# Performance work log

Measured on AMD Instinct MI355X. Metric: run time of the kernel, lower is better.

The kernel has to match this reference:

```python
import jax, jax.numpy as jnp
import numpy as np

T, B, A, H = 128, 32, 6, 128  # rollout len, envs, actions, lstm hidden


def _conv(x, w, b, stride):
    # x: NCHW, w: OIHW (torch layout), VALID padding like nn.Conv2d default
    y = jax.lax.conv_general_dilated(
        x, w, (stride, stride), 'VALID',
        dimension_numbers=('NCHW', 'OIHW', 'NCHW'))
    return y + b[None, :, None, None]


def setup_inputs() -> dict:
    key = jax.random.key(0)
    ks = jax.random.split(key, 12)
    s = 0.05  # weight scale to keep activations in a sane range
    inp = {
        'x': jax.random.uniform(ks[0], (T * B, 1, 84, 84), jnp.float32) * 255.0,
        'done': (jax.random.uniform(ks[1], (T * B,)) < 0.05).astype(jnp.float32),
        'h0': jnp.zeros((1, B, H), jnp.float32),
        'c0': jnp.zeros((1, B, H), jnp.float32),
        'W1': jax.random.normal(ks[2], (32, 1, 8, 8), jnp.float32) * s,
        'b1': jnp.zeros((32,), jnp.float32),
        'W2': jax.random.normal(ks[3], (64, 32, 4, 4), jnp.float32) * s,
        'b2': jnp.zeros((64,), jnp.float32),
        'W3': jax.random.normal(ks[4], (64, 64, 3, 3), jnp.float32) * s,
        'b3': jnp.zeros((64,), jnp.float32),
        'Wfc': jax.random.normal(ks[5], (512, 3136), jnp.float32) * s,
        'bfc': jnp.zeros((512,), jnp.float32),
        'W_ih': jax.random.normal(ks[6], (4 * H, 512), jnp.float32) * s,
        'W_hh': jax.random.normal(ks[7], (4 * H, H), jnp.float32) * s,
        'b_ih': jnp.zeros((4 * H,), jnp.float32),
        'b_hh': jnp.zeros((4 * H,), jnp.float32),
        'Wa': jax.random.normal(ks[8], (A, H), jnp.float32) * 0.01,
        'ba': jnp.zeros((A,), jnp.float32),
        'Wc': jax.random.normal(ks[9], (1, H), jnp.float32) * s,
        'bc': jnp.zeros((1,), jnp.float32),
    }
    return inp


def reference(x, done, h0, c0, W1, b1, W2, b2, W3, b3, Wfc, bfc,
              W_ih, W_hh, b_ih, b_hh, Wa, ba, Wc, bc):
    # --- conv feature extractor (x / 255.0) ---
    z = x / 255.0
    z = jax.nn.relu(_conv(z, W1, b1, 4))   # (N,32,20,20)
    z = jax.nn.relu(_conv(z, W2, b2, 2))   # (N,64,9,9)
    z = jax.nn.relu(_conv(z, W3, b3, 1))   # (N,64,7,7)
    z = z.reshape(z.shape[0], -1)           # (N,3136), torch flatten order
    hidden = jax.nn.relu(z @ Wfc.T + bfc)   # (N,512)

    batch = h0.shape[1]
    xs = hidden.reshape(-1, batch, 512)     # (T,B,512)
    ds = done.reshape(-1, batch)            # (T,B)

    # precompute input projection for all steps at once
    gates_x = jnp.einsum('tbi,gi->tbg', xs, W_ih) + b_ih  # (T,B,4H)

    def step(carry, inp):
        h, c = carry
        gx, d = inp
        mask = (1.0 - d)[:, None]           # reset state where done
        h = h * mask
        c = c * mask
        gates = gx + h @ W_hh.T + b_hh
        i, f, g, o = jnp.split(gates, 4, axis=-1)  # torch gate order i,f,g,o
        c = jax.nn.sigmoid(f) * c + jax.nn.sigmoid(i) * jnp.tanh(g)
        h = jax.nn.sigmoid(o) * jnp.tanh(c)
        return (h, c), h

    (hT, cT), hs = jax.lax.scan(step, (h0[0], c0[0]), (gates_x, ds))
    new_hidden = hs.reshape(-1, hs.shape[-1])  # (T*B, 128)

    logits = new_hidden @ Wa.T + ba            # (T*B, A)
    value = new_hidden @ Wc.T + bc             # (T*B, 1)
    return logits, value, hT[None], cT[None]
```

## Files before the change

### kernel.cpp

```cpp
#include <hip/hip_runtime.h>

#define TT 128
#define BB 32
#define NN (TT*BB)

typedef float f4 __attribute__((ext_vector_type(4)));
typedef float f32x4 __attribute__((ext_vector_type(4)));
typedef short s8 __attribute__((ext_vector_type(8)));
typedef short bf16x8 __attribute__((ext_vector_type(8)));
typedef short s4v __attribute__((ext_vector_type(4)));

__device__ __forceinline__ float bf2f(unsigned short u){
  union{unsigned int i; float f;} x; x.i = ((unsigned int)u)<<16; return x.f;
}
__device__ __forceinline__ unsigned short f2bf(float f){
  union{float ff; unsigned int i;} x; x.ff=f;
  unsigned int r = x.i + 0x7FFFu + ((x.i>>16)&1u);
  return (unsigned short)(r>>16);
}
__device__ __forceinline__ float fsig(float x){
  return __builtin_amdgcn_rcpf(1.f + __expf(-x));
}
__device__ __forceinline__ float ftanh(float x){
  return 1.f - 2.f*__builtin_amdgcn_rcpf(1.f + __expf(2.f*x));
}
__device__ __forceinline__ void gload_lds16(const void* g, void* lds){
  __builtin_amdgcn_global_load_lds(
    (const __attribute__((address_space(1))) unsigned int*)g,
    (__attribute__((address_space(3))) unsigned int*)lds, 16, 0, 0);
}

__global__ __launch_bounds__(256) void prep_w1(const float* __restrict__ W1,
    unsigned short* __restrict__ w1c){
  int i = blockIdx.x*256 + threadIdx.x;
  w1c[i] = f2bf(W1[i] * (1.f/255.f));
}
__global__ __launch_bounds__(256) void prep_w2(const float* __restrict__ W2,
    unsigned short* __restrict__ w2c){
  int i = blockIdx.x*256 + threadIdx.x;
  int co = i >> 9; int rem = i & 511; int khw = rem >> 5; int ci = rem & 31;
  w2c[i] = f2bf(W2[(co*32 + ci)*16 + khw]);
}
__global__ __launch_bounds__(256) void prep_w3(const float* __restrict__ W3,
    unsigned short* __restrict__ w3c){
  int i = blockIdx.x*256 + threadIdx.x;
  int co = i/576; int rem = i - co*576; int khw = rem >> 6; int ci = rem & 63;
  w3c[i] = f2bf(W3[(co*64 + ci)*9 + khw]);
}
__global__ __launch_bounds__(256) void prep_wfc(const float* __restrict__ Wfc,
    unsigned short* __restrict__ wfcc){
  int i = blockIdx.x*256 + threadIdx.x;
  int nn = i/3136; int rem = i - nn*3136; int sp = rem >> 6; int ci = rem & 63;
  wfcc[i] = f2bf(Wfc[nn*3136 + ci*49 + sp]);
}
__global__ __launch_bounds__(256) void prep_wih(const float* __restrict__ W_ih,
    unsigned short* __restrict__ wihc){
  int i = blockIdx.x*256 + threadIdx.x;
  wihc[i] = f2bf(W_ih[i]);
}
__global__ __launch_bounds__(256) void prep_whh(const float* __restrict__ W_hh,
    unsigned short* __restrict__ whhc){
  int i = blockIdx.x*256 + threadIdx.x;
  whhc[i] = f2bf(W_hh[i]);
}

__global__ __launch_bounds__(256) void conv12_k(
    const float* __restrict__ x,
    const unsigned short* __restrict__ w1c, const float* __restrict__ b1,
    const unsigned short* __restrict__ w2c, const float* __restrict__ b2,
    unsigned short* __restrict__ z2){
  __shared__ unsigned short xI[84*88];
  __shared__ unsigned short z1s[200*64];
  __shared__ unsigned short w1L[32*68];
  int t = threadIdx.x;
  int n = blockIdx.x;
  int w = t >> 6, l = t & 63;
  int lr = l & 15, lg = l >> 4;

  {
    bf16x8 v = *(const bf16x8*)&w1c[t*8];
    *(bf16x8*)&w1L[(t>>3)*68 + (t&7)*8] = v;
  }
  {
    const float* xb = x + (size_t)n*7056;
    #pragma unroll
    for(int j=0;j<7;j++){
      int idx = t + 256*j;
      if(idx < 1764){
        f4 v = *(const f4*)(xb + idx*4);
        s4v p;
        #pragma unroll
        for(int e=0;e<4;e++) p[e] = (short)f2bf(v[e]);
        int row = idx/21, col = (idx - row*21)*4;
        *(s4v*)&xI[row*88 + col] = p;
      }
    }
  }
  __syncthreads();

  bf16x8 wf1[2][2];
  #pragma unroll
  for(int nt=0;nt<2;nt++)
    #pragma unroll
    for(int s=0;s<2;s++)
      wf1[nt][s] = *(const bf16x8*)&w1L[(nt*16+lr)*68 + s*32 + lg*8];
  f4 b1v[2];
  b1v[0] = *(const f4*)&b1[lg*4];
  b1v[1] = *(const f4*)&b1[16 + lg*4];
  for(int mt=w; mt<25; mt+=4){
    int p = mt*16 + lr;
    int oh = p/20, ow = p - oh*20;
    bf16x8 a0 = *(const bf16x8*)&xI[(oh*4 + lg    )*88 + ow*4];
    bf16x8 a1 = *(const bf16x8*)&xI[(oh*4 + 4 + lg)*88 + ow*4];
    f32x4 acc[2] = {};
    acc[0] = __builtin_amdgcn_mfma_f32_16x16x32_bf16(wf1[0][0], a0, acc[0], 0,0,0);
    acc[0] = __builtin_amdgcn_mfma_f32_16x16x32_bf16(wf1[0][1], a1, acc[0], 0,0,0);
    acc[1] = __builtin_amdgcn_mfma_f32_16x16x32_bf16(wf1[1][0], a0, acc[1], 0,0,0);
    acc[1] = __builtin_amdgcn_mfma_f32_16x16x32_bf16(wf1[1][1], a1, acc[1], 0,0,0);
    int row = p >> 1;
    int par = (p & 1) << 6;
    int swz = (row & 7) << 4;
    #pragma unroll
    for(int nt=0;nt<2;nt++){
      s4v hp;
      #pragma unroll
      for(int reg=0;reg<4;reg++){
        float v = acc[nt][reg] + b1v[nt][reg];
        v = v>0.f ? v : 0.f;
        hp[reg] = (short)f2bf(v);
      }
      int byteoff = (par + (nt*16 + lg*4)*2) ^ swz;
      *(s4v*)((char*)z1s + row*128 + byteoff) = hp;
    }
  }
  __syncthreads();

  int rbase[6];
  #pragma unroll
  for(int mt=0;mt<6;mt++){
    int q = mt*16 + lr; if(q > 80) q = 80;
    int oh = q/9, ow = q - oh*9;
    rbase[mt] = (2*oh)*20 + 2*ow;
  }
  const unsigned short* wrow = w2c + (size_t)(w*16 + lr)*512 + lg*8;
  bf16x8 bq0 = *(const bf16x8*)(wrow);
  bf16x8 bq1 = *(const bf16x8*)(wrow + 32);
  f32x4 acc2[6] = {};
  #pragma unroll
  for(int s=0;s<16;s++){
    bf16x8 bcur = (s & 1) ? bq1 : bq0;
    if(s+2 < 16){
      bf16x8 bn = *(const bf16x8*)(wrow + (s+2)*32);
      if(s & 1) bq1 = bn; else bq0 = bn;
    }
    int kh = s>>2, kw = s&3;
    int swzbase = ((kw & 1) << 6) + (lg << 4);
    #pragma unroll
    for(int mt=0;mt<6;mt++){
      int p = rbase[mt] + kh*20 + kw;
      int row = p >> 1;
      int byteoff = swzbase ^ ((row & 7) << 4);
      bf16x8 af = *(const bf16x8*)((const char*)z1s + row*128 + byteoff);
      acc2[mt] = __builtin_amdgcn_mfma_f32_16x16x32_bf16(af, bcur, acc2[mt], 0,0,0);
    }
  }
  {
    int ch = w*16 + lr;
    float bb = b2[ch];
    #pragma unroll
    for(int mt=0;mt<6;mt++)
      #pragma unroll
      for(int reg=0;reg<4;reg++){
        int q = mt*16 + lg*4 + reg;
        if(q < 81){
          float v = acc2[mt][reg] + bb; v = v>0.f ? v : 0.f;
          z2[((size_t)n*81 + q)*64 + ch] = f2bf(v);
        }
      }
  }
}

template<int MODE, int OUTBF16, int RELU, int SWZ>
__global__ __launch_bounds__(256) void mgemm_k(
    const unsigned short* __restrict__ A, const unsigned short* __restrict__ B,
    const float* __restrict__ bias1, const float* __restrict__ bias2,
    void* __restrict__ Cout, int K, int Nld, int nout){
  __shared__ unsigned short As[128*40];
  __shared__ unsigned short Bs[64*40];
  int t = threadIdx.x;
  int bm = blockIdx.y, bn = blockIdx.x;
  if(SWZ){
    int cpx = gridDim.y >> 3;
    bm = (bm & 7)*cpx + (bm >> 3);
  }
  int arow = t >> 1, ahalf = t & 1;
  int gm = bm*128 + arow;
  const unsigned short* abase;
  if(MODE == 0){
    abase = A + (size_t)gm*K + ahalf*16;
  } else {
    int n = gm/49; int r = gm - n*49; int oh = r/7; int ow = r - oh*7;
    abase = A + (((size_t)n*9 + oh)*9 + ow)*64 + ahalf*16;
  }
  int brow = t >> 2, bq = t & 3;
  const unsigned short* bbase = B + (size_t)(bn*64 + brow)*K + bq*8;
  int l = t & 63, w = t >> 6;
  int wr = w >> 1, wc = w & 1;
  int lr = l & 15, lk = (l >> 4)*8;
  f32x4 acc[4][2] = {};
  int nsteps = K >> 5;
  for(int s=0; s<nsteps; s++){
    const unsigned short* src;
    if(MODE == 0){
      src = abase + s*32;
    } else {
      int khw = s >> 1; int kh = khw/3; int kw = khw - kh*3;
      src = abase + (kh*9 + kw)*64 + (s & 1)*32;
    }
    bf16x8 a0 = *(const bf16x8*)src;
    bf16x8 a1 = *(const bf16x8*)(src + 8);
    *(bf16x8*)&As[arow*40 + ahalf*16] = a0;
    *(bf16x8*)&As[arow*40 + ahalf*16 + 8] = a1;
    bf16x8 bv = *(const bf16x8*)(bbase + s*32);
    *(bf16x8*)&Bs[brow*40 + bq*8] = bv;
    __syncthreads();
    bf16x8 af[4];
    #pragma unroll
    for(int mf=0; mf<4; mf++)
      af[mf] = *(const bf16x8*)&As[(wr*64 + mf*16 + lr)*40 + lk];
    bf16x8 b0 = *(const bf16x8*)&Bs[(wc*32 + lr)*40 + lk];
    bf16x8 b1 = *(const bf16x8*)&Bs[(wc*32 + 16 + lr)*40 + lk];
    #pragma unroll
    for(int mf=0; mf<4; mf++){
      acc[mf][0] = __builtin_amdgcn_mfma_f32_16x16x32_bf16(af[mf], b0, acc[mf][0], 0, 0, 0);
      acc[mf][1] = __builtin_amdgcn_mfma_f32_16x16x32_bf16(af[mf], b1, acc[mf][1], 0, 0, 0);
    }
    __syncthreads();
  }
  #pragma unroll
  for(int nf=0; nf<2; nf++){
    int gcol = bn*64 + wc*32 + nf*16 + lr;
    if(gcol >= nout) continue;
    float bb = bias1[gcol] + (bias2 ? bias2[gcol] : 0.f);
    #pragma unroll
    for(int mf=0; mf<4; mf++){
      #pragma unroll
      for(int reg=0; reg<4; reg++){
        int grow = bm*128 + wr*64 + mf*16 + (l>>4)*4 + reg;
        float v = acc[mf][nf][reg] + bb;
        if(RELU) v = v>0.f ? v : 0.f;
        if(OUTBF16) ((unsigned short*)Cout)[(size_t)grow*Nld + gcol] = f2bf(v);
        else        ((float*)Cout)[(size_t)grow*Nld + gcol] = v;
      }
    }
  }
}

__global__ __launch_bounds__(512) void lstm_v3_k(
    const float* __restrict__ gx,
    const float* __restrict__ done,
    const float* __restrict__ h0, const float* __restrict__ c0,
    const unsigned short* __restrict__ whhc,
    float* __restrict__ hs, float* __restrict__ out_hT, float* __restrict__ out_cT){
  __shared__ float mask_lds[TT*4];
  __shared__ unsigned short hA[2][4][136];
  __shared__ __align__(16) float gxS[3][4][520];
  __shared__ __align__(16) float gW[8][256];
  int tid = threadIdx.x;
  int B0 = blockIdx.x * 4;
  int w = tid >> 6, l = tid & 63;
  int lr = l & 15, lg = l >> 4;
  int cu = 16*w + (l >> 2);
  int cb = l & 3;
  int drow = w >> 1, dhalf = w & 1;

  bf16x8 wA[4][4];
  #pragma unroll
  for(int g=0; g<4; g++)
    #pragma unroll
    for(int kt=0; kt<4; kt++)
      wA[g][kt] = *(const bf16x8*)&whhc[(size_t)(g*128 + 16*w + lr)*128 + kt*32 + lg*8];

  {
    int tt = tid >> 2, bb = tid & 3;
    mask_lds[tid] = 1.f - done[tt*32 + B0 + bb];
  }
  float cv = c0[(size_t)(B0+cb)*128 + cu];
  float hv0 = h0[(size_t)(B0+cb)*128 + cu];
  float hout = 0.f;
  {
    float m0 = 1.f - done[0*BB + B0 + cb];
    hA[0][cb][cu] = f2bf(hv0 * m0);
  }
  #pragma unroll
  for(int sl=0; sl<2; sl++)
    gload_lds16(gx + ((size_t)(sl*32 + B0 + drow))*512 + dhalf*256 + l*4,
                &gxS[sl][drow][dhalf*256]);
  __syncthreads();

  int slot = 0;
  for(int t=0; t<TT; t++){
    int cur = t & 1;
    {
      int ts = (t+2 < TT) ? t+2 : TT-1;
      int s2 = (slot >= 1) ? slot-1 : 2;
      gload_lds16(gx + ((size_t)(ts*32 + B0 + drow))*512 + dhalf*256 + l*4,
                  &gxS[s2][drow][dhalf*256]);
    }
    bf16x8 hF[4];
    #pragma unroll
    for(int kt=0; kt<4; kt++)
      hF[kt] = *(const bf16x8*)&hA[cur][lr & 3][kt*32 + lg*8];
    f32x4 acc[4] = {};
    #pragma unroll
    for(int kt=0; kt<4; kt++)
      #pragma unroll
      for(int g=0; g<4; g++)
        acc[g] = __builtin_amdgcn_mfma_f32_16x16x32_bf16(wA[g][kt], hF[kt], acc[g], 0, 0, 0);
    if(lr < 4){
      #pragma unroll
      for(int g=0; g<4; g++)
        #pragma unroll
        for(int r=0; r<4; r++)
          gW[w][g*64 + (lg*4 + r)*4 + lr] = acc[g][r];
    }
    asm volatile("s_waitcnt lgkmcnt(0)" ::: "memory");
    float g0 = gW[w][      l];
    float g1 = gW[w][ 64 + l];
    float g2 = gW[w][128 + l];
    float g3 = gW[w][192 + l];
    float gx0 = gxS[slot][cb][      cu];
    float gx1 = gxS[slot][cb][128 + cu];
    float gx2 = gxS[slot][cb][256 + cu];
    float gx3 = gxS[slot][cb][384 + cu];
    float m  = mask_lds[t*4 + cb];
    float mn = (t < TT-1) ? mask_lds[(t+1)*4 + cb] : 1.f;
    float iv = fsig (g0 + gx0);
    float fv = fsig (g1 + gx1);
    float gv = ftanh(g2 + gx2);
    float ov = fsig (g3 + gx3);
    float cn = fv*(cv*m) + iv*gv;
    float hn = ov*ftanh(cn);
    cv = cn; hout = hn;
    hs[((size_t)t*BB + B0 + cb)*128 + cu] = hn;
    hA[cur^1][cb][cu] = f2bf(hn * mn);
    asm volatile("s_waitcnt vmcnt(3) lgkmcnt(0)" ::: "memory");
    __builtin_amdgcn_s_barrier();
    slot = (slot >= 2) ? 0 : slot+1;
  }
  out_hT[(size_t)(B0+cb)*128 + cu] = hout;
  out_cT[(size_t)(B0+cb)*128 + cu] = cv;
}

__global__ __launch_bounds__(256) void heads_k(const float* __restrict__ hs,
    const float* __restrict__ Wa, const float* __restrict__ ba,
    const float* __restrict__ Wc, const float* __restrict__ bc,
    float* __restrict__ out){
  int gid = blockIdx.x*256 + threadIdx.x;
  int n = gid/7, a = gid - n*7;
  const float* w = (a<6) ? (Wa + a*128) : Wc;
  float bias = (a<6) ? ba[a] : bc[0];
  const float* h = hs + (size_t)n*128;
  float acc = 0.f;
  #pragma unroll
  for(int k=0;k<32;k++){
    f4 hv = *(const f4*)(h + k*4);
    f4 wv = *(const f4*)(w + k*4);
    acc += hv[0]*wv[0]+hv[1]*wv[1]+hv[2]*wv[2]+hv[3]*wv[3];
  }
  float v = acc + bias;
  if(a<6) out[(size_t)n*6 + a] = v;
  else    out[24576 + n] = v;
}

extern "C" void kernel_launch(void* const* d_in, const int* in_sizes, int n_in,
                              void* d_out, int out_size, void* d_ws, size_t ws_size,
                              hipStream_t stream){
  const float* x    = (const float*)d_in[0];
  const float* done = (const float*)d_in[1];
  const float* h0   = (const float*)d_in[2];
  const float* c0   = (const float*)d_in[3];
  const float* W1   = (const float*)d_in[4];
  const float* b1   = (const float*)d_in[5];
  const float* W2   = (const float*)d_in[6];
  const float* b2   = (const float*)d_in[7];
  const float* W3   = (const float*)d_in[8];
  const float* b3   = (const float*)d_in[9];
  const float* Wfc  = (const float*)d_in[10];
  const float* bfc  = (const float*)d_in[11];
  const float* W_ih = (const float*)d_in[12];
  const float* W_hh = (const float*)d_in[13];
  const float* b_ih = (const float*)d_in[14];
  const float* b_hh = (const float*)d_in[15];
  const float* Wa   = (const float*)d_in[16];
  const float* ba   = (const float*)d_in[17];
  const float* Wc   = (const float*)d_in[18];
  const float* bc   = (const float*)d_in[19];
  float* out = (float*)d_out;

  char* ws = (char*)d_ws;
  unsigned short* z2   = (unsigned short*)(ws + 0);
  unsigned short* z3   = (unsigned short*)(ws + 42467328);
  unsigned short* hid  = (unsigned short*)(ws + 68157440);
  float* gx            = (float*)(ws + 72351744);
  float* hs            = (float*)(ws + 80740352);
  unsigned short* w1c  = (unsigned short*)(ws + 82837504);
  unsigned short* w2c  = (unsigned short*)(ws + 82845696);
  unsigned short* w3c  = (unsigned short*)(ws + 82911232);
  unsigned short* wfcc = (unsigned short*)(ws + 82984960);
  unsigned short* wihc = (unsigned short*)(ws + 86196224);
  unsigned short* whhc = (unsigned short*)(ws + 86720512);

  prep_w1 <<<8,   256, 0, stream>>>(W1, w1c);
  prep_w2 <<<128, 256, 0, stream>>>(W2, w2c);
  prep_w3 <<<144, 256, 0, stream>>>(W3, w3c);
  prep_wfc<<<6272,256, 0, stream>>>(Wfc, wfcc);
  prep_wih<<<1024,256, 0, stream>>>(W_ih, wihc);
  prep_whh<<<256, 256, 0, stream>>>(W_hh, whhc);

  conv12_k<<<4096,256,0,stream>>>(x, w1c, b1, w2c, b2, z2);
  mgemm_k<2,1,1,1><<<dim3(1,1568),256,0,stream>>>(z2, w3c, b3, nullptr, z3, 576, 64, 64);
  mgemm_k<0,1,1,0><<<dim3(8,32),256,0,stream>>>(z3, wfcc, bfc, nullptr, hid, 3136, 512, 512);
  mgemm_k<0,0,0,0><<<dim3(8,32),256,0,stream>>>(hid, wihc, b_ih, b_hh, gx, 512, 512, 512);

  lstm_v3_k<<<8,512,0,stream>>>(gx, done, h0, c0, whhc, hs, out+28672, out+32768);
  heads_k<<<112,256,0,stream>>>(hs, Wa, ba, Wc, bc, out);
}
```

Measured before the change: 305.1 us.

## Fuse conv3 into per-image conv kernel and merge weight-prep launches

The conv3 implicit GEMM moves into the per-image conv kernel, so conv2 output stays in a swizzled LDS buffer (aliased over the input image) and never goes to global memory. Conv2 and conv3 are reorganised so each wave computes two 16-channel output tiles over a subset of spatial tiles, with weights as the A operand and activations as B. The six weight-prep kernels become one launch. This removes the z2 global round trip (~42MB) and several launches, at the cost of more LDS reuse pressure and extra per-block work in the conv kernel.

```diff
diff --git a/kernel.cpp b/kernel.cpp
--- a/kernel.cpp
+++ b/kernel.cpp
@@ -30,52 +30,51 @@
     (__attribute__((address_space(3))) unsigned int*)lds, 16, 0, 0);
 }
 
-__global__ __launch_bounds__(256) void prep_w1(const float* __restrict__ W1,
-    unsigned short* __restrict__ w1c){
+__global__ __launch_bounds__(256) void prep_all(
+    const float* __restrict__ W1, const float* __restrict__ W2,
+    const float* __restrict__ W3, const float* __restrict__ Wfc,
+    const float* __restrict__ W_ih, const float* __restrict__ W_hh,
+    unsigned short* __restrict__ w1c, unsigned short* __restrict__ w2c,
+    unsigned short* __restrict__ w3c, unsigned short* __restrict__ wfcc,
+    unsigned short* __restrict__ wihc, unsigned short* __restrict__ whhc){
   int i = blockIdx.x*256 + threadIdx.x;
-  w1c[i] = f2bf(W1[i] * (1.f/255.f));
-}
-__global__ __launch_bounds__(256) void prep_w2(const float* __restrict__ W2,
-    unsigned short* __restrict__ w2c){
-  int i = blockIdx.x*256 + threadIdx.x;
-  int co = i >> 9; int rem = i & 511; int khw = rem >> 5; int ci = rem & 31;
-  w2c[i] = f2bf(W2[(co*32 + ci)*16 + khw]);
-}
-__global__ __launch_bounds__(256) void prep_w3(const float* __restrict__ W3,
-    unsigned short* __restrict__ w3c){
-  int i = blockIdx.x*256 + threadIdx.x;
-  int co = i/576; int rem = i - co*576; int khw = rem >> 6; int ci = rem & 63;
-  w3c[i] = f2bf(W3[(co*64 + ci)*9 + khw]);
-}
-__global__ __launch_bounds__(256) void prep_wfc(const float* __restrict__ Wfc,
-    unsigned short* __restrict__ wfcc){
-  int i = blockIdx.x*256 + threadIdx.x;
-  int nn = i/3136; int rem = i - nn*3136; int sp = rem >> 6; int ci = rem & 63;
-  wfcc[i] = f2bf(Wfc[nn*3136 + ci*49 + sp]);
-}
-__global__ __launch_bounds__(256) void prep_wih(const float* __restrict__ W_ih,
-    unsigned short* __restrict__ wihc){
-  int i = blockIdx.x*256 + threadIdx.x;
-  wihc[i] = f2bf(W_ih[i]);
-}
-__global__ __launch_bounds__(256) void prep_whh(const float* __restrict__ W_hh,
-    unsigned short* __restrict__ whhc){
-  int i = blockIdx.x*256 + threadIdx.x;
-  whhc[i] = f2bf(W_hh[i]);
-}
-
-__global__ __launch_bounds__(256) void conv12_k(
+  if(i < 1605632){
+    int nn = i/3136; int rem = i - nn*3136; int sp = rem >> 6; int ci = rem & 63;
+    wfcc[i] = f2bf(Wfc[nn*3136 + ci*49 + sp]); return;
+  }
+  i -= 1605632;
+  if(i < 262144){ wihc[i] = f2bf(W_ih[i]); return; }
+  i -= 262144;
+  if(i < 65536){ whhc[i] = f2bf(W_hh[i]); return; }
+  i -= 65536;
+  if(i < 36864){
+    int co = i/576; int rem = i - co*576; int khw = rem >> 6; int ci = rem & 63;
+    w3c[i] = f2bf(W3[(co*64 + ci)*9 + khw]); return;
+  }
+  i -= 36864;
+  if(i < 32768){
+    int co = i >> 9; int rem = i & 511; int khw = rem >> 5; int ci = rem & 31;
+    w2c[i] = f2bf(W2[(co*32 + ci)*16 + khw]); return;
+  }
+  i -= 32768;
+  if(i < 2048){ w1c[i] = f2bf(W1[i] * (1.f/255.f)); }
+}
+
+__global__ __launch_bounds__(256) void conv123_k(
     const float* __restrict__ x,
     const unsigned short* __restrict__ w1c, const float* __restrict__ b1,
     const unsigned short* __restrict__ w2c, const float* __restrict__ b2,
-    unsigned short* __restrict__ z2){
-  __shared__ unsigned short xI[84*88];
-  __shared__ unsigned short z1s[200*64];
-  __shared__ unsigned short w1L[32*68];
-  int t = threadIdx.x;
-  int n = blockIdx.x;
+    const unsigned short* __restrict__ w3c, const float* __restrict__ b3,
+    unsigned short* __restrict__ z3){
+  __shared__ __align__(16) char smem[44736];
+  unsigned short* w1L = (unsigned short*)(smem + 25600);
+  unsigned short* xI  = (unsigned short*)(smem + 29952);
+  char* z2s = smem + 29952;
+  int t = threadIdx.x, n = blockIdx.x;
   int w = t >> 6, l = t & 63;
   int lr = l & 15, lg = l >> 4;
+  int ch2 = w >> 1;
+  int mj  = w & 1;
 
   {
     bf16x8 v = *(const bf16x8*)&w1c[t*8];
@@ -84,8 +83,8 @@
   {
     const float* xb = x + (size_t)n*7056;
     #pragma unroll
-    for(int j=0;j<7;j++){
-      int idx = t + 256*j;
+    for(int jj=0;jj<7;jj++){
+      int idx = t + 256*jj;
       if(idx < 1764){
         f4 v = *(const f4*)(xb + idx*4);
         s4v p;
@@ -98,110 +97,162 @@
   }
   __syncthreads();
 
-  bf16x8 wf1[2][2];
-  #pragma unroll
-  for(int nt=0;nt<2;nt++)
-    #pragma unroll
-    for(int s=0;s<2;s++)
-      wf1[nt][s] = *(const bf16x8*)&w1L[(nt*16+lr)*68 + s*32 + lg*8];
-  f4 b1v[2];
-  b1v[0] = *(const f4*)&b1[lg*4];
-  b1v[1] = *(const f4*)&b1[16 + lg*4];
-  for(int mt=w; mt<25; mt+=4){
-    int p = mt*16 + lr;
-    int oh = p/20, ow = p - oh*20;
-    bf16x8 a0 = *(const bf16x8*)&xI[(oh*4 + lg    )*88 + ow*4];
-    bf16x8 a1 = *(const bf16x8*)&xI[(oh*4 + 4 + lg)*88 + ow*4];
-    f32x4 acc[2] = {};
-    acc[0] = __builtin_amdgcn_mfma_f32_16x16x32_bf16(wf1[0][0], a0, acc[0], 0,0,0);
-    acc[0] = __builtin_amdgcn_mfma_f32_16x16x32_bf16(wf1[0][1], a1, acc[0], 0,0,0);
-    acc[1] = __builtin_amdgcn_mfma_f32_16x16x32_bf16(wf1[1][0], a0, acc[1], 0,0,0);
-    acc[1] = __builtin_amdgcn_mfma_f32_16x16x32_bf16(wf1[1][1], a1, acc[1], 0,0,0);
-    int row = p >> 1;
-    int par = (p & 1) << 6;
-    int swz = (row & 7) << 4;
-    #pragma unroll
-    for(int nt=0;nt<2;nt++){
-      s4v hp;
-      #pragma unroll
-      for(int reg=0;reg<4;reg++){
-        float v = acc[nt][reg] + b1v[nt][reg];
-        v = v>0.f ? v : 0.f;
-        hp[reg] = (short)f2bf(v);
-      }
-      int byteoff = (par + (nt*16 + lg*4)*2) ^ swz;
-      *(s4v*)((char*)z1s + row*128 + byteoff) = hp;
+  {
+    bf16x8 wf1[2][2];
+    #pragma unroll
+    for(int nt=0;nt<2;nt++)
+      #pragma unroll
+      for(int s=0;s<2;s++)
+        wf1[nt][s] = *(const bf16x8*)&w1L[(nt*16+lr)*68 + s*32 + lg*8];
+    f4 b1v[2];
+    b1v[0] = *(const f4*)&b1[lg*4];
+    b1v[1] = *(const f4*)&b1[16 + lg*4];
+    for(int mt=w; mt<25; mt+=4){
+      int p = mt*16 + lr;
+      int oh = p/20, ow = p - oh*20;
+      bf16x8 a0 = *(const bf16x8*)&xI[(oh*4 + lg    )*88 + ow*4];
+      bf16x8 a1 = *(const bf16x8*)&xI[(oh*4 + 4 + lg)*88 + ow*4];
+      f32x4 acc[2] = {};
+      acc[0] = __builtin_amdgcn_mfma_f32_16x16x32_bf16(wf1[0][0], a0, acc[0], 0,0,0);
+      acc[0] = __builtin_amdgcn_mfma_f32_16x16x32_bf16(wf1[0][1], a1, acc[0], 0,0,0);
+      acc[1] = __builtin_amdgcn_mfma_f32_16x16x32_bf16(wf1[1][0], a0, acc[1], 0,0,0);
+      acc[1] = __builtin_amdgcn_mfma_f32_16x16x32_bf16(wf1[1][1], a1, acc[1], 0,0,0);
+      int row = p >> 1, par = (p & 1) << 6, swz = (row & 7) << 4;
+      #pragma unroll
+      for(int nt=0;nt<2;nt++){
+        s4v hp;
+        #pragma unroll
+        for(int reg=0;reg<4;reg++){
+          float v = acc[nt][reg] + b1v[nt][reg];
+          v = v>0.f ? v : 0.f;
+          hp[reg] = (short)f2bf(v);
+        }
+        int bo = (par + (nt*16 + lg*4)*2) ^ swz;
+        *(s4v*)(smem + row*128 + bo) = hp;
+      }
     }
   }
   __syncthreads();
 
-  int rbase[6];
-  #pragma unroll
-  for(int mt=0;mt<6;mt++){
-    int q = mt*16 + lr; if(q > 80) q = 80;
-    int oh = q/9, ow = q - oh*9;
-    rbase[mt] = (2*oh)*20 + 2*ow;
-  }
-  const unsigned short* wrow = w2c + (size_t)(w*16 + lr)*512 + lg*8;
-  bf16x8 bq0 = *(const bf16x8*)(wrow);
-  bf16x8 bq1 = *(const bf16x8*)(wrow + 32);
-  f32x4 acc2[6] = {};
-  #pragma unroll
-  for(int s=0;s<16;s++){
-    bf16x8 bcur = (s & 1) ? bq1 : bq0;
-    if(s+2 < 16){
-      bf16x8 bn = *(const bf16x8*)(wrow + (s+2)*32);
-      if(s & 1) bq1 = bn; else bq0 = bn;
-    }
-    int kh = s>>2, kw = s&3;
-    int swzbase = ((kw & 1) << 6) + (lg << 4);
-    #pragma unroll
-    for(int mt=0;mt<6;mt++){
-      int p = rbase[mt] + kh*20 + kw;
-      int row = p >> 1;
-      int byteoff = swzbase ^ ((row & 7) << 4);
-      bf16x8 af = *(const bf16x8*)((const char*)z1s + row*128 + byteoff);
-      acc2[mt] = __builtin_amdgcn_mfma_f32_16x16x32_bf16(af, bcur, acc2[mt], 0,0,0);
-    }
-  }
-  {
-    int ch = w*16 + lr;
-    float bb = b2[ch];
-    #pragma unroll
-    for(int mt=0;mt<6;mt++)
-      #pragma unroll
-      for(int reg=0;reg<4;reg++){
-        int q = mt*16 + lg*4 + reg;
-        if(q < 81){
-          float v = acc2[mt][reg] + bb; v = v>0.f ? v : 0.f;
-          z2[((size_t)n*81 + q)*64 + ch] = f2bf(v);
+  {
+    int rb2[3];
+    #pragma unroll
+    for(int m=0;m<3;m++){
+      int q = (3*mj+m)*16 + lr; if(q > 80) q = 80;
+      int oh = q/9, ow = q - oh*9;
+      rb2[m] = 2*oh*20 + 2*ow;
+    }
+    const unsigned short* w2p0 = w2c + (size_t)((2*ch2  )*16+lr)*512 + lg*8;
+    const unsigned short* w2p1 = w2c + (size_t)((2*ch2+1)*16+lr)*512 + lg*8;
+    bf16x8 aq0[2], aq1[2];
+    aq0[0] = *(const bf16x8*)w2p0;      aq1[0] = *(const bf16x8*)w2p1;
+    aq0[1] = *(const bf16x8*)(w2p0+32); aq1[1] = *(const bf16x8*)(w2p1+32);
+    f32x4 acc2[3][2] = {};
+    #pragma unroll
+    for(int s=0;s<16;s++){
+      bf16x8 a0 = aq0[s&1], a1 = aq1[s&1];
+      if(s+2 < 16){
+        aq0[s&1] = *(const bf16x8*)(w2p0 + (s+2)*32);
+        aq1[s&1] = *(const bf16x8*)(w2p1 + (s+2)*32);
+      }
+      int kh = s>>2, kw = s&3;
+      #pragma unroll
+      for(int m=0;m<3;m++){
+        int p = rb2[m] + kh*20 + kw;
+        int row = p >> 1;
+        int bo = (((p&1)<<6) + (lg<<4)) ^ ((row&7)<<4);
+        bf16x8 bf = *(const bf16x8*)(smem + row*128 + bo);
+        acc2[m][0] = __builtin_amdgcn_mfma_f32_16x16x32_bf16(a0, bf, acc2[m][0], 0,0,0);
+        acc2[m][1] = __builtin_amdgcn_mfma_f32_16x16x32_bf16(a1, bf, acc2[m][1], 0,0,0);
+      }
+    }
+    f4 b2v0 = *(const f4*)&b2[(2*ch2  )*16 + lg*4];
+    f4 b2v1 = *(const f4*)&b2[(2*ch2+1)*16 + lg*4];
+    #pragma unroll
+    for(int m=0;m<3;m++){
+      int q = (3*mj+m)*16 + lr;
+      if(q < 81){
+        int swz = (q & 7) << 4;
+        s4v h0p, h1p;
+        #pragma unroll
+        for(int reg=0;reg<4;reg++){
+          float v0 = acc2[m][0][reg] + b2v0[reg]; v0 = v0>0.f ? v0 : 0.f;
+          float v1 = acc2[m][1][reg] + b2v1[reg]; v1 = v1>0.f ? v1 : 0.f;
+          h0p[reg] = (short)f2bf(v0);
+          h1p[reg] = (short)f2bf(v1);
         }
-      }
-  }
-}
-
-template<int MODE, int OUTBF16, int RELU, int SWZ>
+        *(s4v*)(z2s + q*128 + (((2*ch2  )*32 + lg*8) ^ swz)) = h0p;
+        *(s4v*)(z2s + q*128 + (((2*ch2+1)*32 + lg*8) ^ swz)) = h1p;
+      }
+    }
+  }
+  __syncthreads();
+
+  {
+    int rb3[2];
+    #pragma unroll
+    for(int m=0;m<2;m++){
+      int q = (2*mj+m)*16 + lr; if(q > 48) q = 48;
+      int oh = q/7, ow = q - oh*7;
+      rb3[m] = oh*9 + ow;
+    }
+    const unsigned short* w3p0 = w3c + (size_t)((2*ch2  )*16+lr)*576 + lg*8;
+    const unsigned short* w3p1 = w3c + (size_t)((2*ch2+1)*16+lr)*576 + lg*8;
+    bf16x8 cq0[2], cq1[2];
+    cq0[0] = *(const bf16x8*)w3p0;      cq1[0] = *(const bf16x8*)w3p1;
+    cq0[1] = *(const bf16x8*)(w3p0+32); cq1[1] = *(const bf16x8*)(w3p1+32);
+    f32x4 acc3[2][2] = {};
+    #pragma unroll
+    for(int s=0;s<18;s++){
+      bf16x8 a0 = cq0[s&1], a1 = cq1[s&1];
+      if(s+2 < 18){
+        cq0[s&1] = *(const bf16x8*)(w3p0 + (s+2)*32);
+        cq1[s&1] = *(const bf16x8*)(w3p1 + (s+2)*32);
+      }
+      int khw = s>>1; int kh = khw/3, kw = khw - kh*3;
+      int cb = (s&1)<<6;
+      #pragma unroll
+      for(int m=0;m<2;m++){
+        int pp = rb3[m] + kh*9 + kw;
+        int bo = (cb + (lg<<4)) ^ ((pp&7)<<4);
+        bf16x8 bf = *(const bf16x8*)(z2s + pp*128 + bo);
+        acc3[m][0] = __builtin_amdgcn_mfma_f32_16x16x32_bf16(a0, bf, acc3[m][0], 0,0,0);
+        acc3[m][1] = __builtin_amdgcn_mfma_f32_16x16x32_bf16(a1, bf, acc3[m][1], 0,0,0);
+      }
+    }
+    f4 b3v0 = *(const f4*)&b3[(2*ch2  )*16 + lg*4];
+    f4 b3v1 = *(const f4*)&b3[(2*ch2+1)*16 + lg*4];
+    unsigned short* zo = z3 + (size_t)n*3136;
+    #pragma unroll
+    for(int m=0;m<2;m++){
+      int q = (2*mj+m)*16 + lr;
+      if(q < 49){
+        s4v h0p, h1p;
+        #pragma unroll
+        for(int reg=0;reg<4;reg++){
+          float v0 = acc3[m][0][reg] + b3v0[reg]; v0 = v0>0.f ? v0 : 0.f;
+          float v1 = acc3[m][1][reg] + b3v1[reg]; v1 = v1>0.f ? v1 : 0.f;
+          h0p[reg] = (short)f2bf(v0);
+          h1p[reg] = (short)f2bf(v1);
+        }
+        *(s4v*)&zo[q*64 + (2*ch2  )*16 + lg*4] = h0p;
+        *(s4v*)&zo[q*64 + (2*ch2+1)*16 + lg*4] = h1p;
+      }
+    }
+  }
+}
+
+template<int OUTBF16, int RELU>
 __global__ __launch_bounds__(256) void mgemm_k(
     const unsigned short* __restrict__ A, const unsigned short* __restrict__ B,
     const float* __restrict__ bias1, const float* __restrict__ bias2,
-    void* __restrict__ Cout, int K, int Nld, int nout){
+    void* __restrict__ Cout, int K, int Nld){
   __shared__ unsigned short As[128*40];
   __shared__ unsigned short Bs[64*40];
   int t = threadIdx.x;
   int bm = blockIdx.y, bn = blockIdx.x;
-  if(SWZ){
-    int cpx = gridDim.y >> 3;
-    bm = (bm & 7)*cpx + (bm >> 3);
-  }
   int arow = t >> 1, ahalf = t & 1;
-  int gm = bm*128 + arow;
-  const unsigned short* abase;
-  if(MODE == 0){
-    abase = A + (size_t)gm*K + ahalf*16;
-  } else {
-    int n = gm/49; int r = gm - n*49; int oh = r/7; int ow = r - oh*7;
-    abase = A + (((size_t)n*9 + oh)*9 + ow)*64 + ahalf*16;
-  }
+  const unsigned short* abase = A + (size_t)(bm*128+arow)*K + ahalf*16;
   int brow = t >> 2, bq = t & 3;
   const unsigned short* bbase = B + (size_t)(bn*64 + brow)*K + bq*8;
   int l = t & 63, w = t >> 6;
@@ -210,13 +261,7 @@
   f32x4 acc[4][2] = {};
   int nsteps = K >> 5;
   for(int s=0; s<nsteps; s++){
-    const unsigned short* src;
-    if(MODE == 0){
-      src = abase + s*32;
-    } else {
-      int khw = s >> 1; int kh = khw/3; int kw = khw - kh*3;
-      src = abase + (kh*9 + kw)*64 + (s & 1)*32;
-    }
+    const unsigned short* src = abase + s*32;
     bf16x8 a0 = *(const bf16x8*)src;
     bf16x8 a1 = *(const bf16x8*)(src + 8);
     *(bf16x8*)&As[arow*40 + ahalf*16] = a0;
@@ -240,7 +285,6 @@
   #pragma unroll
   for(int nf=0; nf<2; nf++){
     int gcol = bn*64 + wc*32 + nf*16 + lr;
-    if(gcol >= nout) continue;
     float bb = bias1[gcol] + (bias2 ? bias2[gcol] : 0.f);
     #pragma unroll
     for(int mf=0; mf<4; mf++){
@@ -399,29 +443,22 @@
   float* out = (float*)d_out;
 
   char* ws = (char*)d_ws;
-  unsigned short* z2   = (unsigned short*)(ws + 0);
-  unsigned short* z3   = (unsigned short*)(ws + 42467328);
-  unsigned short* hid  = (unsigned short*)(ws + 68157440);
-  float* gx            = (float*)(ws + 72351744);
-  float* hs            = (float*)(ws + 80740352);
-  unsigned short* w1c  = (unsigned short*)(ws + 82837504);
-  unsigned short* w2c  = (unsigned short*)(ws + 82845696);
-  unsigned short* w3c  = (unsigned short*)(ws + 82911232);
-  unsigned short* wfcc = (unsigned short*)(ws + 82984960);
-  unsigned short* wihc = (unsigned short*)(ws + 86196224);
-  unsigned short* whhc = (unsigned short*)(ws + 86720512);
-
-  prep_w1 <<<8,   256, 0, stream>>>(W1, w1c);
-  prep_w2 <<<128, 256, 0, stream>>>(W2, w2c);
-  prep_w3 <<<144, 256, 0, stream>>>(W3, w3c);
-  prep_wfc<<<6272,256, 0, stream>>>(Wfc, wfcc);
-  prep_wih<<<1024,256, 0, stream>>>(W_ih, wihc);
-  prep_whh<<<256, 256, 0, stream>>>(W_hh, whhc);
-
-  conv12_k<<<4096,256,0,stream>>>(x, w1c, b1, w2c, b2, z2);
-  mgemm_k<2,1,1,1><<<dim3(1,1568),256,0,stream>>>(z2, w3c, b3, nullptr, z3, 576, 64, 64);
-  mgemm_k<0,1,1,0><<<dim3(8,32),256,0,stream>>>(z3, wfcc, bfc, nullptr, hid, 3136, 512, 512);
-  mgemm_k<0,0,0,0><<<dim3(8,32),256,0,stream>>>(hid, wihc, b_ih, b_hh, gx, 512, 512, 512);
+  unsigned short* z3   = (unsigned short*)(ws + 0);
+  unsigned short* hid  = (unsigned short*)(ws + 25690112);
+  float* gx            = (float*)(ws + 29884416);
+  float* hs            = (float*)(ws + 38273024);
+  unsigned short* w1c  = (unsigned short*)(ws + 40370176);
+  unsigned short* w2c  = (unsigned short*)(ws + 40374272);
+  unsigned short* w3c  = (unsigned short*)(ws + 40439808);
+  unsigned short* wfcc = (unsigned short*)(ws + 40513536);
+  unsigned short* wihc = (unsigned short*)(ws + 43724800);
+  unsigned short* whhc = (unsigned short*)(ws + 44249088);
+
+  prep_all<<<7832,256,0,stream>>>(W1, W2, W3, Wfc, W_ih, W_hh,
+                                  w1c, w2c, w3c, wfcc, wihc, whhc);
+  conv123_k<<<4096,256,0,stream>>>(x, w1c, b1, w2c, b2, w3c, b3, z3);
+  mgemm_k<1,1><<<dim3(8,32),256,0,stream>>>(z3, wfcc, bfc, nullptr, hid, 3136, 512);
+  mgemm_k<0,0><<<dim3(8,32),256,0,stream>>>(hid, wihc, b_ih, b_hh, gx, 512, 512);
 
   lstm_v3_k<<<8,512,0,stream>>>(gx, done, h0, c0, whhc, hs, out+28672, out+32768);
   heads_k<<<112,256,0,stream>>>(hs, Wa, ba, Wc, bc, out);
```

Result: slower. 371.7 us (+21.8%).
